# Kernel optimization log

Measured on AMD Instinct MI355X. Metric: run time of the kernel, lower is better.

Reference implementation:

```python
import jax, jax.numpy as jnp
import numpy as np
import math

H = 1024
N = 64
DT_MIN, DT_MAX = 1e-3, 1e-1
L_SEQ = 4096


def setup_inputs() -> dict:
    key = jax.random.key(0)
    k1, k2, k3 = jax.random.split(key, 3)
    # C ~ complex normal, stored as (..., 2) real view like torch.view_as_real
    C = jax.random.normal(k1, (H, N // 2, 2), dtype=jnp.float32)
    # log_dt ~ U[log(dt_min), log(dt_max)]
    log_dt = jax.random.uniform(k2, (H,), dtype=jnp.float32) * (
        math.log(DT_MAX) - math.log(DT_MIN)
    ) + math.log(DT_MIN)
    # log_A_real = log(0.5), A_imag = pi * arange(N/2) repeated over H
    log_A_real = jnp.full((H, N // 2), math.log(0.5), dtype=jnp.float32)
    A_imag = math.pi * jnp.broadcast_to(
        jnp.arange(N // 2, dtype=jnp.float32), (H, N // 2)
    )
    return {"C": C, "log_dt": log_dt, "log_A_real": log_A_real, "A_imag": A_imag, "L": L_SEQ}


def reference(C, log_dt, log_A_real, A_imag, L):
    dt = jnp.exp(log_dt)                                  # (H,)
    Cc = jax.lax.complex(C[..., 0], C[..., 1])            # (H, N/2) complex
    A = -jnp.exp(log_A_real) + 1j * A_imag                # (H, N/2) complex
    dtA = A * dt[:, None]                                 # (H, N/2)
    # Vandermonde: exp(dtA * l) for l in [0, L)
    K = dtA[:, :, None] * jnp.arange(L, dtype=jnp.float32)  # (H, N/2, L)
    Cm = Cc * (jnp.exp(dtA) - 1.0) / A                    # (H, N/2)
    K = 2.0 * jnp.einsum("hn,hnl->hl", Cm, jnp.exp(K)).real  # (H, L)
    return K
```

## Files before the change

kernel.cpp:

```cpp
#include <hip/hip_runtime.h>
#include <hip/hip_bf16.h>
#include <math.h>


#define H_DIM 1024
#define NH 32
#define L_DIM 4096
#define TPB 256
#define CHUNK 8
#define STRIDE_F 72

typedef float v2f __attribute__((ext_vector_type(2)));

#if defined(__has_builtin) && __has_builtin(__builtin_elementwise_fma)
#define V2FMA(a, b, c) __builtin_elementwise_fma((a), (b), (c))
#else
#define V2FMA(a, b, c) ((a) * (b) + (c))
#endif

__global__ __launch_bounds__(TPB, 4) void s4d_kernel(
    const float* __restrict__ C,
    const float* __restrict__ log_dt,
    const float* __restrict__ log_A_real,
    const float* __restrict__ A_imag,
    float* __restrict__ out)
{
    const int h = blockIdx.x;
    const int t = threadIdx.x;

    __shared__ float lds[NH * STRIDE_F];

    const double INV_2PI = 0.15915494309189533576888376337251;

    {
        const int n = t & 31;
        const int s = t >> 5;

        const float dtf = __expf(log_dt[h]);
        const float arf = -__expf(log_A_real[h * NH + n]);
        const float aif = A_imag[h * NH + n];
        const float are = arf * dtf;
        const double th_rev = (double)aif * (double)dtf * INV_2PI;

        const float mw = __expf(are);
        const float u1 = (float)(th_rev - floor(th_rev));
        const float wr = mw * __builtin_amdgcn_cosf(u1);
        const float wi = mw * __builtin_amdgcn_sinf(u1);

        const float cr = C[(h * NH + n) * 2 + 0];
        const float ci = C[(h * NH + n) * 2 + 1];
        const float er = wr - 1.0f;
        const float ei = wi;
        const float tr = cr * er - ci * ei;
        const float ti = cr * ei + ci * er;
        const float inv = 2.0f / (arf * arf + aif * aif);
        const float cmr = (tr * arf + ti * aif) * inv;
        const float cmi = (ti * arf - tr * aif) * inv;

        float* base = &lds[n * STRIDE_F];

#pragma unroll
        for (int k = 0; k < 2; ++k) {
            const int i = s + 8 * k;
            const int l = 16 * i;
            const float mag = __expf(are * (float)l);
            double u = (double)l * th_rev;
            u -= floor(u);
            const float uf = (float)u;
            const float br = mag * __builtin_amdgcn_cosf(uf);
            const float bi = mag * __builtin_amdgcn_sinf(uf);
            base[6 + 2 * i]     = cmr * br - cmi * bi;
            base[6 + 2 * i + 1] = cmr * bi + cmi * br;
        }
#pragma unroll
        for (int k = 0; k < 2; ++k) {
            const int i = s + 8 * k;
            const int l = 256 * i;
            const float mag = __expf(are * (float)l);
            double u = (double)l * th_rev;
            u -= floor(u);
            const float uf = (float)u;
            base[38 + 2 * i]     = mag * __builtin_amdgcn_cosf(uf);
            base[38 + 2 * i + 1] = mag * __builtin_amdgcn_sinf(uf);
        }
        if (s == 0) {
            base[0] = wr;
            base[1] = wi;
            base[2] = wr + wr;
            base[3] = -__expf(are + are);
            const float m8 = __expf(are * 8.0f);
            double u8 = th_rev * 8.0;
            u8 -= floor(u8);
            const float uf8 = (float)u8;
            base[4] = m8 * __builtin_amdgcn_cosf(uf8);
            base[5] = m8 * __builtin_amdgcn_sinf(uf8);
        }
    }
    __syncthreads();

    v2f acc[CHUNK];
#pragma unroll
    for (int j = 0; j < CHUNK; ++j) acc[j] = (v2f){0.0f, 0.0f};

    const int ia = t & 15;
    const int ib = t >> 4;

#pragma unroll 4
    for (int n = 0; n < NH; ++n) {
        const float* base = &lds[n * STRIDE_F];
        const float4 h4 = *(const float4*)base;
        const float2 w8 = *(const float2*)(base + 4);
        const float2 ta = *(const float2*)(base + 6 + 2 * ia);
        const float2 tb = *(const float2*)(base + 38 + 2 * ib);

        const float zr  = ta.x * tb.x - ta.y * tb.y;
        const float zi  = ta.x * tb.y + ta.y * tb.x;
        const float zbr = zr * w8.x - zi * w8.y;
        const float zbi = zr * w8.y + zi * w8.x;

        v2f x0 = {zr, zbr};
        v2f x1 = {zr * h4.x - zi * h4.y, zbr * h4.x - zbi * h4.y};
        acc[0] += x0;
        acc[1] += x1;
        const v2f p2 = {h4.z, h4.z};
        const v2f q2 = {h4.w, h4.w};
        v2f tq = q2 * x0;
#pragma unroll
        for (int j = 2; j < CHUNK; ++j) {
            const v2f x2 = V2FMA(p2, x1, tq);
            tq = q2 * x1;
            acc[j] += x2;
            x1 = x2;
        }
    }

    float4* op = (float4*)(out + (size_t)h * L_DIM + t * 16);
    op[0] = make_float4(acc[0].x, acc[1].x, acc[2].x, acc[3].x);
    op[1] = make_float4(acc[4].x, acc[5].x, acc[6].x, acc[7].x);
    op[2] = make_float4(acc[0].y, acc[1].y, acc[2].y, acc[3].y);
    op[3] = make_float4(acc[4].y, acc[5].y, acc[6].y, acc[7].y);
}

extern "C" void kernel_launch(void* const* d_in, const int* in_sizes, int n_in,
                              void* d_out, int out_size, void* d_ws, size_t ws_size,
                              hipStream_t stream) {
    const float* C          = (const float*)d_in[0];
    const float* log_dt     = (const float*)d_in[1];
    const float* log_A_real = (const float*)d_in[2];
    const float* A_imag     = (const float*)d_in[3];
    float* out = (float*)d_out;

    s4d_kernel<<<dim3(H_DIM), dim3(TPB), 0, stream>>>(C, log_dt, log_A_real, A_imag, out);
}
```

Baseline: 76.86 us.

## Process two heads per block with 32 outputs per thread via longer recurrence

Each block now handles two heads, with 128 threads per head, and each thread produces 32 consecutive outputs instead of 16. Each thread runs a 16-step second-order recurrence on two interleaved seeds. The starting values for both seeds (offset by 16, plus the next element) are precomputed into shared memory, so the inner loop no longer does the per-n complex multiplies for the second-seed and first-step setup. This removes per-mode setup work per output and halves the block count. In exchange it uses more registers (launch bounds lowered to 2), longer recurrence chains that may lose accuracy, and a larger shared-memory footprint.

```diff
diff --git a/kernel.cpp b/kernel.cpp
--- a/kernel.cpp
+++ b/kernel.cpp
@@ -7,8 +7,8 @@
 #define NH 32
 #define L_DIM 4096
 #define TPB 256
-#define CHUNK 8
-#define STRIDE_F 72
+#define NSTEP 16
+#define STRIDE_F 160
 
 typedef float v2f __attribute__((ext_vector_type(2)));
 
@@ -18,23 +18,25 @@
 #define V2FMA(a, b, c) ((a) * (b) + (c))
 #endif
 
-__global__ __launch_bounds__(TPB, 4) void s4d_kernel(
+__global__ __launch_bounds__(TPB, 2) void s4d_kernel(
     const float* __restrict__ C,
     const float* __restrict__ log_dt,
     const float* __restrict__ log_A_real,
     const float* __restrict__ A_imag,
     float* __restrict__ out)
 {
-    const int h = blockIdx.x;
-    const int t = threadIdx.x;
+    const int t  = threadIdx.x;
+    const int hh = t >> 7;
+    const int u  = t & 127;
+    const int h  = 2 * blockIdx.x + hh;
 
-    __shared__ float lds[NH * STRIDE_F];
+    __shared__ float lds[2 * NH * STRIDE_F];
 
     const double INV_2PI = 0.15915494309189533576888376337251;
 
     {
-        const int n = t & 31;
-        const int s = t >> 5;
+        const int n = u & 31;
+        const int s = u >> 5;
 
         const float dtf = __expf(log_dt[h]);
         const float arf = -__expf(log_A_real[h * NH + n]);
@@ -47,6 +49,12 @@
         const float wr = mw * __builtin_amdgcn_cosf(u1);
         const float wi = mw * __builtin_amdgcn_sinf(u1);
 
+        const float m16 = __expf(are * 16.0f);
+        double u16 = th_rev * 16.0;
+        u16 -= floor(u16);
+        const float w16r = m16 * __builtin_amdgcn_cosf((float)u16);
+        const float w16i = m16 * __builtin_amdgcn_sinf((float)u16);
+
         const float cr = C[(h * NH + n) * 2 + 0];
         const float ci = C[(h * NH + n) * 2 + 1];
         const float er = wr - 1.0f;
@@ -57,76 +65,79 @@
         const float cmr = (tr * arf + ti * aif) * inv;
         const float cmi = (ti * arf - tr * aif) * inv;
 
-        float* base = &lds[n * STRIDE_F];
+        const float p = wr + wr;
+        const float q = -__expf(are + are);
+
+        float* base = &lds[(hh * NH + n) * STRIDE_F];
 
 #pragma unroll
-        for (int k = 0; k < 2; ++k) {
-            const int i = s + 8 * k;
-            const int l = 16 * i;
+        for (int k = 0; k < 4; ++k) {
+            const int i = s + 4 * k;
+            const int l = 32 * i;
             const float mag = __expf(are * (float)l);
-            double u = (double)l * th_rev;
-            u -= floor(u);
-            const float uf = (float)u;
-            const float br = mag * __builtin_amdgcn_cosf(uf);
-            const float bi = mag * __builtin_amdgcn_sinf(uf);
-            base[6 + 2 * i]     = cmr * br - cmi * bi;
-            base[6 + 2 * i + 1] = cmr * bi + cmi * br;
+            double uu = (double)l * th_rev;
+            uu -= floor(uu);
+            const float pr = mag * __builtin_amdgcn_cosf((float)uu);
+            const float pi = mag * __builtin_amdgcn_sinf((float)uu);
+            const float e0r = cmr * pr - cmi * pi;
+            const float e0i = cmr * pi + cmi * pr;
+            const float e1r = e0r * wr - e0i * wi;
+            const float e1i = e0r * wi + e0i * wr;
+            const float f0r = e0r * w16r - e0i * w16i;
+            const float f0i = e0r * w16i + e0i * w16r;
+            const float f1r = f0r * wr - f0i * wi;
+            const float f1i = f0r * wi + f0i * wr;
+            float* p8 = base + 8 * i;
+            p8[0] = e0r; p8[1] = e0i; p8[2] = e1r; p8[3] = e1i;
+            p8[4] = f0r; p8[5] = f0i; p8[6] = f1r; p8[7] = f1i;
         }
 #pragma unroll
         for (int k = 0; k < 2; ++k) {
-            const int i = s + 8 * k;
-            const int l = 256 * i;
+            const int b = s + 4 * k;
+            const int l = 512 * b;
             const float mag = __expf(are * (float)l);
-            double u = (double)l * th_rev;
-            u -= floor(u);
-            const float uf = (float)u;
-            base[38 + 2 * i]     = mag * __builtin_amdgcn_cosf(uf);
-            base[38 + 2 * i + 1] = mag * __builtin_amdgcn_sinf(uf);
-        }
-        if (s == 0) {
-            base[0] = wr;
-            base[1] = wi;
-            base[2] = wr + wr;
-            base[3] = -__expf(are + are);
-            const float m8 = __expf(are * 8.0f);
-            double u8 = th_rev * 8.0;
-            u8 -= floor(u8);
-            const float uf8 = (float)u8;
-            base[4] = m8 * __builtin_amdgcn_cosf(uf8);
-            base[5] = m8 * __builtin_amdgcn_sinf(uf8);
+            double uu = (double)l * th_rev;
+            uu -= floor(uu);
+            float* p4 = base + 128 + 4 * b;
+            p4[0] = mag * __builtin_amdgcn_cosf((float)uu);
+            p4[1] = mag * __builtin_amdgcn_sinf((float)uu);
+            p4[2] = p;
+            p4[3] = q;
         }
     }
     __syncthreads();
 
-    v2f acc[CHUNK];
+    v2f acc[NSTEP];
 #pragma unroll
-    for (int j = 0; j < CHUNK; ++j) acc[j] = (v2f){0.0f, 0.0f};
+    for (int j = 0; j < NSTEP; ++j) acc[j] = (v2f){0.0f, 0.0f};
 
-    const int ia = t & 15;
-    const int ib = t >> 4;
+    const int a = u & 15;
+    const int b = u >> 4;
 
-#pragma unroll 4
+    const float* hbase = &lds[hh * NH * STRIDE_F];
+
+#pragma unroll 2
     for (int n = 0; n < NH; ++n) {
-        const float* base = &lds[n * STRIDE_F];
-        const float4 h4 = *(const float4*)base;
-        const float2 w8 = *(const float2*)(base + 4);
-        const float2 ta = *(const float2*)(base + 6 + 2 * ia);
-        const float2 tb = *(const float2*)(base + 38 + 2 * ib);
+        const float* base = hbase + n * STRIDE_F;
+        const float4 ta0 = *(const float4*)(base + 8 * a);
+        const float4 ta1 = *(const float4*)(base + 8 * a + 4);
+        const float4 tb  = *(const float4*)(base + 128 + 4 * b);
 
-        const float zr  = ta.x * tb.x - ta.y * tb.y;
-        const float zi  = ta.x * tb.y + ta.y * tb.x;
-        const float zbr = zr * w8.x - zi * w8.y;
-        const float zbi = zr * w8.y + zi * w8.x;
+        const float x0A = ta0.x * tb.x - ta0.y * tb.y;
+        const float x1A = ta0.z * tb.x - ta0.w * tb.y;
+        const float x0B = ta1.x * tb.x - ta1.y * tb.y;
+        const float x1B = ta1.z * tb.x - ta1.w * tb.y;
 
-        v2f x0 = {zr, zbr};
-        v2f x1 = {zr * h4.x - zi * h4.y, zbr * h4.x - zbi * h4.y};
+        v2f x1 = {x1A, x1B};
+        const v2f x0 = {x0A, x0B};
+        const v2f p2 = {tb.z, tb.z};
+        const v2f q2 = {tb.w, tb.w};
+
         acc[0] += x0;
         acc[1] += x1;
-        const v2f p2 = {h4.z, h4.z};
-        const v2f q2 = {h4.w, h4.w};
         v2f tq = q2 * x0;
 #pragma unroll
-        for (int j = 2; j < CHUNK; ++j) {
+        for (int j = 2; j < NSTEP; ++j) {
             const v2f x2 = V2FMA(p2, x1, tq);
             tq = q2 * x1;
             acc[j] += x2;
@@ -134,11 +145,14 @@
         }
     }
 
-    float4* op = (float4*)(out + (size_t)h * L_DIM + t * 16);
-    op[0] = make_float4(acc[0].x, acc[1].x, acc[2].x, acc[3].x);
-    op[1] = make_float4(acc[4].x, acc[5].x, acc[6].x, acc[7].x);
-    op[2] = make_float4(acc[0].y, acc[1].y, acc[2].y, acc[3].y);
-    op[3] = make_float4(acc[4].y, acc[5].y, acc[6].y, acc[7].y);
+    float4* op = (float4*)(out + (size_t)h * L_DIM + 32 * u);
+#pragma unroll
+    for (int k = 0; k < 4; ++k) {
+        op[k]     = make_float4(acc[4 * k].x, acc[4 * k + 1].x,
+                                acc[4 * k + 2].x, acc[4 * k + 3].x);
+        op[4 + k] = make_float4(acc[4 * k].y, acc[4 * k + 1].y,
+                                acc[4 * k + 2].y, acc[4 * k + 3].y);
+    }
 }
 
 extern "C" void kernel_launch(void* const* d_in, const int* in_sizes, int n_in,
@@ -150,5 +164,5 @@
     const float* A_imag     = (const float*)d_in[3];
     float* out = (float*)d_out;
 
-    s4d_kernel<<<dim3(H_DIM), dim3(TPB), 0, stream>>>(C, log_dt, log_A_real, A_imag, out);
+    s4d_kernel<<<dim3(H_DIM / 2), dim3(TPB), 0, stream>>>(C, log_dt, log_A_real, A_imag, out);
 }
```

Result: no change. 78.10 us (+1.6%).
